# Optimization experiments

Hardware: AMD Instinct MI355X
Metric: run time of the kernel (lower is better)

The kernel has to match this reference:

```python
import jax, jax.numpy as jnp
import numpy as np

J = 4
K = 16  # kernel_size
M_ORDER = 4
PAD = K // 2


def _make_filters():
    t = np.linspace(-2.0, 2.0, K)
    z = 1.0 - 1j * t
    psi = (1.0 / z) ** (M_ORDER + 1)
    psi = psi - psi.mean()
    phi = np.exp(-2.0 * t ** 2)
    phi = phi / phi.sum()
    psi = psi / np.linalg.norm(psi) / np.sqrt(2.0)
    phi = phi / np.linalg.norm(phi) / np.sqrt(2.0)
    return (psi.real.astype(np.float32), psi.imag.astype(np.float32),
            phi.astype(np.float32))


def setup_inputs() -> dict:
    key = jax.random.key(0)
    k1, k2 = jax.random.split(key)
    B, T = 32, 524288
    x_real = jax.random.normal(k1, (B, T), dtype=jnp.float32)
    x_imag = jax.random.normal(k2, (B, T), dtype=jnp.float32)
    pr, pi, ph = _make_filters()
    return {
        'x_real': x_real, 'x_imag': x_imag,
        'psi_real': jnp.asarray(pr), 'psi_imag': jnp.asarray(pi),
        'phi': jnp.asarray(ph),
    }


def _conv_same(x, w, L):
    # x: (B, L) real; w: (K,) real. torch F.conv1d = cross-correlation, 'same'-ish
    # padding K//2 gives length L+1, trimmed back to L (as in the torch code).
    y = jax.lax.conv_general_dilated(x[:, None, :], w[None, None, :],
                                     window_strides=(1,),
                                     padding=[(PAD, PAD)])
    return y[:, 0, :L]


def reference(x_real, x_imag, psi_real, psi_imag, phi):
    x = x_real + 1j * x_imag  # complex64
    coefficients = []
    for j in range(J):
        L = x.shape[-1]
        xr, xi = x.real, x.imag
        # low-pass (complex signal * real filter), then decimate by 2
        s = _conv_same(xr, phi, L) + 1j * _conv_same(xi, phi, L)
        coefficients.append(s[..., ::2])
        # complex band-pass conv: (a+bi)*(c+di)
        rr = _conv_same(xr, psi_real, L)
        ri = _conv_same(xr, psi_imag, L)
        ir = _conv_same(xi, psi_real, L)
        ii = _conv_same(xi, psi_imag, L)
        u = (rr - ii) + 1j * (ri + ir)
        # modulus rectifier (cast back to complex, imag = 0)
        w = jnp.abs(u).astype(u.dtype)
        x = w[..., ::2]
        if x.shape[-1] < K:
            break
    return tuple(coefficients)
```

## Files before the change

### kernel.cpp

```cpp
#include <hip/hip_runtime.h>


using f16x2 = __attribute__((ext_vector_type(2))) __fp16;

static __device__ __forceinline__ uint packh2(float a, float b) {
    f16x2 r = __builtin_amdgcn_cvt_pkrtz(a, b);
    return __builtin_bit_cast(uint, r);
}
static __device__ __forceinline__ float dot2(f16x2 f, uint w, float c) {
#if __has_builtin(__builtin_amdgcn_fdot2)
    return __builtin_amdgcn_fdot2(f, __builtin_bit_cast(f16x2, w), c, false);
#else
    f16x2 h = __builtin_bit_cast(f16x2, w);
    return fmaf((float)f.x, (float)h.x, fmaf((float)f.y, (float)h.y, c));
#endif
}

constexpr int S1   = 1024;
constexpr int H1   = 56;
constexpr int NT1  = S1 + 2 * H1;
constexpr int NPIN = 1144;
constexpr int NLD  = NPIN / 2;
constexpr int NTH  = 256;

__global__ __launch_bounds__(NTH, 6) void hst_fused_kernel(
    const float* __restrict__ xr, const float* __restrict__ xi,
    const float* __restrict__ psi_r, const float* __restrict__ psi_i,
    const float* __restrict__ phi,
    float* __restrict__ out,
    long o0, long o1, long o2, long o3,
    int L0, int h0, int h1, int h2, int h3)
{
    __shared__ __align__(16) uint REP[NPIN];
    __shared__ __align__(16) uint IMP[NPIN];
    __shared__ __align__(16) uint X1P[572];
    __shared__ __align__(16) uint X2P[284];
    __shared__ __align__(16) uint X3P[136];

    const int tid  = threadIdx.x;
    const int wv   = tid >> 6;
    const int lane = tid & 63;
    const int gx   = blockIdx.x;
    const int b    = blockIdx.y;
    const int s    = gx * S1;
    const bool edge = (gx == 0) || (gx == (int)gridDim.x - 1);
    const int X0   = 2 * (s - H1) - 8;

    const float* rowr = xr + (size_t)b * (size_t)L0;
    const float* rowi = xi + (size_t)b * (size_t)L0;

    f16x2 FH[8], FR[8], FI[8];
    #pragma unroll
    for (int j = 0; j < 8; ++j) {
        FH[j] = __builtin_amdgcn_cvt_pkrtz(phi[2*j],   phi[2*j+1]);
        FR[j] = __builtin_amdgcn_cvt_pkrtz(psi_r[2*j], psi_r[2*j+1]);
        FI[j] = __builtin_amdgcn_cvt_pkrtz(psi_i[2*j], psi_i[2*j+1]);
    }

    if (!edge) {
        const float4* pr4 = reinterpret_cast<const float4*>(rowr + X0);
        const float4* pi4 = reinterpret_cast<const float4*>(rowi + X0);
        #pragma unroll
        for (int n = 0; n < 2; ++n) {
            const int i = tid + n * NTH;
            float4 a = pr4[i];
            float4 c = pi4[i];
            uint2 wa; wa.x = packh2(a.x, a.y); wa.y = packh2(a.z, a.w);
            uint2 wc; wc.x = packh2(c.x, c.y); wc.y = packh2(c.z, c.w);
            *reinterpret_cast<uint2*>(&REP[2*i]) = wa;
            *reinterpret_cast<uint2*>(&IMP[2*i]) = wc;
        }
        if (lane < 15) {
            const int i = 512 + 4 * lane + wv;
            if (i < NLD) {
                float4 a = pr4[i];
                float4 c = pi4[i];
                uint2 wa; wa.x = packh2(a.x, a.y); wa.y = packh2(a.z, a.w);
                uint2 wc; wc.x = packh2(c.x, c.y); wc.y = packh2(c.z, c.w);
                *reinterpret_cast<uint2*>(&REP[2*i]) = wa;
                *reinterpret_cast<uint2*>(&IMP[2*i]) = wc;
            }
        }
    } else {
        for (int i = tid; i < NPIN; i += NTH) {
            int g0 = X0 + 2 * i;
            float r0 = (g0   >= 0 && g0   < L0) ? rowr[g0]   : 0.0f;
            float r1 = (g0+1 >= 0 && g0+1 < L0) ? rowr[g0+1] : 0.0f;
            float i0 = (g0   >= 0 && g0   < L0) ? rowi[g0]   : 0.0f;
            float i1 = (g0+1 >= 0 && g0+1 < L0) ? rowi[g0+1] : 0.0f;
            REP[i] = packh2(r0, r1);
            IMP[i] = packh2(i0, i1);
        }
    }
    __syncthreads();

    {
        const int g = tid;
        const uint4* wp = reinterpret_cast<const uint4*>(&REP[4*g]);
        uint4 a0 = wp[0], a1 = wp[1], a2 = wp[2];
        const uint4* ip = reinterpret_cast<const uint4*>(&IMP[4*g]);
        uint4 c0v = ip[0], c1v = ip[1], c2v = ip[2];
        const uint wr[12] = {a0.x,a0.y,a0.z,a0.w, a1.x,a1.y,a1.z,a1.w, a2.x,a2.y,a2.z,a2.w};
        const uint wi[12] = {c0v.x,c0v.y,c0v.z,c0v.w, c1v.x,c1v.y,c1v.z,c1v.w, c2v.x,c2v.y,c2v.z,c2v.w};

        float phv[4], mag[4];
        #pragma unroll
        for (int r = 0; r < 4; ++r) {
            float sh = 0.f, rr = 0.f, ri = 0.f, ir = 0.f, ii = 0.f;
            #pragma unroll
            for (int j = 0; j < 8; ++j) {
                sh = dot2(FH[j], wr[r+j], sh);
                rr = dot2(FR[j], wr[r+j], rr);
                ri = dot2(FI[j], wr[r+j], ri);
                ir = dot2(FR[j], wi[r+j], ir);
                ii = dot2(FI[j], wi[r+j], ii);
            }
            float ur = rr - ii, ui = ri + ir;
            float m2 = sqrtf(fmaf(ur, ur, ui * ui));
            if (edge) {
                int m = s - H1 + 4*g + r;
                m2 = (m >= 0 && m < h0) ? m2 : 0.0f;
            }
            mag[r] = m2;
            phv[r] = sh;
        }
        uint2 xp; xp.x = packh2(mag[0], mag[1]); xp.y = packh2(mag[2], mag[3]);
        *reinterpret_cast<uint2*>(&X1P[2*g]) = xp;

        if (g >= 14) {
            long m0 = (long)s - H1 + 4*g;
            float4 st; st.x = phv[0]; st.y = phv[1]; st.z = phv[2]; st.w = phv[3];
            *reinterpret_cast<float4*>(out + o0 + (long)b * h0 + m0) = st;
        }
    }

    if (lane < 28) {
        const int h  = 4 * lane + wv;
        const int lm = 1024 + h;
        uint wr8[8], wi8[8];
        #pragma unroll
        for (int j = 0; j < 8; ++j) { wr8[j] = REP[lm + j]; wi8[j] = IMP[lm + j]; }
        float sh = 0.f, rr = 0.f, ri = 0.f, ir = 0.f, ii = 0.f;
        #pragma unroll
        for (int j = 0; j < 8; ++j) {
            sh = dot2(FH[j], wr8[j], sh);
            rr = dot2(FR[j], wr8[j], rr);
            ri = dot2(FI[j], wr8[j], ri);
            ir = dot2(FR[j], wi8[j], ir);
            ii = dot2(FI[j], wi8[j], ii);
        }
        float ur = rr - ii, ui = ri + ir;
        float m2 = sqrtf(fmaf(ur, ur, ui * ui));
        if (edge) {
            int m = s - H1 + lm;
            m2 = (m >= 0 && m < h0) ? m2 : 0.0f;
        }
        reinterpret_cast<__fp16*>(X1P)[lm] = (__fp16)m2;
        if (h < 56)
            out[o0 + (long)b * h0 + (s + 968 + h)] = sh;
    }
    __syncthreads();

    {
        const int t = tid;
        uint2 u0 = *reinterpret_cast<const uint2*>(&X1P[2*t]);
        uint2 u1 = *reinterpret_cast<const uint2*>(&X1P[2*t+2]);
        uint2 u2 = *reinterpret_cast<const uint2*>(&X1P[2*t+4]);
        uint2 u3 = *reinterpret_cast<const uint2*>(&X1P[2*t+6]);
        uint  w8 = X1P[2*t+8];
        const uint w[9] = {u0.x,u0.y,u1.x,u1.y,u2.x,u2.y,u3.x,u3.y,w8};

        float phv[2], mag[2];
        #pragma unroll
        for (int r = 0; r < 2; ++r) {
            float sh = 0.f, ur = 0.f, ui = 0.f;
            #pragma unroll
            for (int j = 0; j < 8; ++j) {
                sh = dot2(FH[j], w[r+j], sh);
                ur = dot2(FR[j], w[r+j], ur);
                ui = dot2(FI[j], w[r+j], ui);
            }
            float m2 = sqrtf(fmaf(ur, ur, ui * ui));
            const int q = s/2 - 24 + 2*t + r;
            if (edge) m2 = (q >= 0 && q < h1) ? m2 : 0.0f;
            mag[r] = m2;
            phv[r] = sh;
        }
        X2P[t] = packh2(mag[0], mag[1]);
        if (t >= 12) {
            long q0 = (long)s/2 - 24 + 2*t;
            *reinterpret_cast<float2*>(out + o1 + (long)b * h1 + q0) =
                make_float2(phv[0], phv[1]);
        }
    }
    if (lane < 12) {
        const int h   = 4 * lane + wv;
        const int pos = 512 + h;
        uint w8[8];
        #pragma unroll
        for (int j = 0; j < 8; ++j) w8[j] = X1P[pos + j];
        float sh = 0.f, ur = 0.f, ui = 0.f;
        #pragma unroll
        for (int j = 0; j < 8; ++j) {
            sh = dot2(FH[j], w8[j], sh);
            ur = dot2(FR[j], w8[j], ur);
            ui = dot2(FI[j], w8[j], ui);
        }
        float m2 = sqrtf(fmaf(ur, ur, ui * ui));
        const int q = s/2 - 24 + pos;
        if (edge) m2 = (q >= 0 && q < h1) ? m2 : 0.0f;
        reinterpret_cast<__fp16*>(X2P)[pos] = (__fp16)m2;
        if (h < 24)
            out[o1 + (long)b * h1 + q] = sh;
    }
    __syncthreads();

    if (tid < 136) {
        const int t = tid;
        uint2 u0 = *reinterpret_cast<const uint2*>(&X2P[2*t]);
        uint2 u1 = *reinterpret_cast<const uint2*>(&X2P[2*t+2]);
        uint2 u2 = *reinterpret_cast<const uint2*>(&X2P[2*t+4]);
        uint2 u3 = *reinterpret_cast<const uint2*>(&X2P[2*t+6]);
        uint  w8 = X2P[2*t+8];
        const uint w[9] = {u0.x,u0.y,u1.x,u1.y,u2.x,u2.y,u3.x,u3.y,w8};

        float phv[2], mag[2];
        #pragma unroll
        for (int r = 0; r < 2; ++r) {
            float sh = 0.f, ur = 0.f, ui = 0.f;
            #pragma unroll
            for (int j = 0; j < 8; ++j) {
                sh = dot2(FH[j], w[r+j], sh);
                ur = dot2(FR[j], w[r+j], ur);
                ui = dot2(FI[j], w[r+j], ui);
            }
            float m2 = sqrtf(fmaf(ur, ur, ui * ui));
            const int p = s/4 - 8 + 2*t + r;
            if (edge) m2 = (p >= 0 && p < h2) ? m2 : 0.0f;
            mag[r] = m2;
            phv[r] = sh;
        }
        X3P[t] = packh2(mag[0], mag[1]);
        if (t >= 4 && t < 132) {
            long p0 = (long)s/4 - 8 + 2*t;
            *reinterpret_cast<float2*>(out + o2 + (long)b * h2 + p0) =
                make_float2(phv[0], phv[1]);
        }
    }
    __syncthreads();

    if (tid < S1/8) {
        float sh = 0.f;
        #pragma unroll
        for (int j = 0; j < 8; ++j)
            sh = dot2(FH[j], X3P[tid + j], sh);
        out[o3 + (long)b * h3 + (s/8 + tid)] = sh;
    }
}

extern "C" void kernel_launch(void* const* d_in, const int* in_sizes, int n_in,
                              void* d_out, int out_size, void* d_ws, size_t ws_size,
                              hipStream_t stream) {
    const float* xr    = (const float*)d_in[0];
    const float* xi    = (const float*)d_in[1];
    const float* psi_r = (const float*)d_in[2];
    const float* psi_i = (const float*)d_in[3];
    const float* phi   = (const float*)d_in[4];
    float* out = (float*)d_out;

    const int B  = 32;
    const int T  = in_sizes[0] / B;
    const int L0 = T;
    const int h0 = L0 / 2;
    const int h1 = h0 / 2;
    const int h2 = h1 / 2;
    const int h3 = h2 / 2;

    const long o0 = 0;
    const long o1 = o0 + (long)B * h0;
    const long o2 = o1 + (long)B * h1;
    const long o3 = o2 + (long)B * h2;

    dim3 blk(NTH, 1, 1);
    dim3 grd(h0 / S1, B, 1);
    hipLaunchKernelGGL(hst_fused_kernel, grd, blk, 0, stream,
                       xr, xi, psi_r, psi_i, phi,
                       out, o0, o1, o2, o3,
                       L0, h0, h1, h2, h3);
}
```

Baseline: 49.32 us.

## Double per-block tile to 2048 samples to amortize halo recomputation

Doubles the output tile per block from 1024 to 2048 samples and enlarges the shared buffers, so each thread now computes two groups in level 1 and four outputs in level 2. The halo cost across the cascaded levels (56 at level 1, 24 at level 2, 8 at level 3) is spread over twice as much useful work, cutting redundant loads and recomputation. The tail-handling thread mappings are reworked for the new sizes. In exchange the grid is half as large, and the larger shared memory footprint and register pressure may lower occupancy.

After: 47.37 us. 4.0% less time.

```diff
diff --git a/kernel.cpp b/kernel.cpp
--- a/kernel.cpp
+++ b/kernel.cpp
@@ -16,11 +16,13 @@
 #endif
 }
 
-constexpr int S1   = 1024;
+constexpr int S1   = 2048;
 constexpr int H1   = 56;
 constexpr int NT1  = S1 + 2 * H1;
-constexpr int NPIN = 1144;
+constexpr int NPIN = 2168;
 constexpr int NLD  = NPIN / 2;
+constexpr int NT2  = S1 / 2 + 48;
+constexpr int NT3  = S1 / 4 + 16;
 constexpr int NTH  = 256;
 
 __global__ __launch_bounds__(NTH, 6) void hst_fused_kernel(
@@ -33,9 +35,9 @@
 {
     __shared__ __align__(16) uint REP[NPIN];
     __shared__ __align__(16) uint IMP[NPIN];
-    __shared__ __align__(16) uint X1P[572];
-    __shared__ __align__(16) uint X2P[284];
-    __shared__ __align__(16) uint X3P[136];
+    __shared__ __align__(16) uint X1P[1080];
+    __shared__ __align__(16) uint X2P[536];
+    __shared__ __align__(16) uint X3P[264];
 
     const int tid  = threadIdx.x;
     const int wv   = tid >> 6;
@@ -61,7 +63,7 @@
         const float4* pr4 = reinterpret_cast<const float4*>(rowr + X0);
         const float4* pi4 = reinterpret_cast<const float4*>(rowi + X0);
         #pragma unroll
-        for (int n = 0; n < 2; ++n) {
+        for (int n = 0; n < 4; ++n) {
             const int i = tid + n * NTH;
             float4 a = pr4[i];
             float4 c = pi4[i];
@@ -71,15 +73,13 @@
             *reinterpret_cast<uint2*>(&IMP[2*i]) = wc;
         }
         if (lane < 15) {
-            const int i = 512 + 4 * lane + wv;
-            if (i < NLD) {
-                float4 a = pr4[i];
-                float4 c = pi4[i];
-                uint2 wa; wa.x = packh2(a.x, a.y); wa.y = packh2(a.z, a.w);
-                uint2 wc; wc.x = packh2(c.x, c.y); wc.y = packh2(c.z, c.w);
-                *reinterpret_cast<uint2*>(&REP[2*i]) = wa;
-                *reinterpret_cast<uint2*>(&IMP[2*i]) = wc;
-            }
+            const int i = 1024 + 15 * wv + lane;
+            float4 a = pr4[i];
+            float4 c = pi4[i];
+            uint2 wa; wa.x = packh2(a.x, a.y); wa.y = packh2(a.z, a.w);
+            uint2 wc; wc.x = packh2(c.x, c.y); wc.y = packh2(c.z, c.w);
+            *reinterpret_cast<uint2*>(&REP[2*i]) = wa;
+            *reinterpret_cast<uint2*>(&IMP[2*i]) = wc;
         }
     } else {
         for (int i = tid; i < NPIN; i += NTH) {
@@ -94,8 +94,9 @@
     }
     __syncthreads();
 
-    {
-        const int g = tid;
+    #pragma unroll
+    for (int n = 0; n < 2; ++n) {
+        const int g = tid + n * NTH;
         const uint4* wp = reinterpret_cast<const uint4*>(&REP[4*g]);
         uint4 a0 = wp[0], a1 = wp[1], a2 = wp[2];
         const uint4* ip = reinterpret_cast<const uint4*>(&IMP[4*g]);
@@ -135,8 +136,8 @@
     }
 
     if (lane < 28) {
-        const int h  = 4 * lane + wv;
-        const int lm = 1024 + h;
+        const int h  = 28 * wv + lane;
+        const int lm = S1 + h;
         uint wr8[8], wi8[8];
         #pragma unroll
         for (int j = 0; j < 8; ++j) { wr8[j] = REP[lm + j]; wi8[j] = IMP[lm + j]; }
@@ -157,22 +158,21 @@
         }
         reinterpret_cast<__fp16*>(X1P)[lm] = (__fp16)m2;
         if (h < 56)
-            out[o0 + (long)b * h0 + (s + 968 + h)] = sh;
+            out[o0 + (long)b * h0 + (s + S1 - H1 + h)] = sh;
     }
     __syncthreads();
 
     {
         const int t = tid;
-        uint2 u0 = *reinterpret_cast<const uint2*>(&X1P[2*t]);
-        uint2 u1 = *reinterpret_cast<const uint2*>(&X1P[2*t+2]);
-        uint2 u2 = *reinterpret_cast<const uint2*>(&X1P[2*t+4]);
-        uint2 u3 = *reinterpret_cast<const uint2*>(&X1P[2*t+6]);
-        uint  w8 = X1P[2*t+8];
-        const uint w[9] = {u0.x,u0.y,u1.x,u1.y,u2.x,u2.y,u3.x,u3.y,w8};
-
-        float phv[2], mag[2];
-        #pragma unroll
-        for (int r = 0; r < 2; ++r) {
+        const uint4* wp = reinterpret_cast<const uint4*>(&X1P[4*t]);
+        uint4 a0 = wp[0], a1 = wp[1];
+        uint2 u2 = *reinterpret_cast<const uint2*>(&X1P[4*t+8]);
+        uint  w10 = X1P[4*t+10];
+        const uint w[11] = {a0.x,a0.y,a0.z,a0.w, a1.x,a1.y,a1.z,a1.w, u2.x,u2.y, w10};
+
+        float phv[4], mag[4];
+        #pragma unroll
+        for (int r = 0; r < 4; ++r) {
             float sh = 0.f, ur = 0.f, ui = 0.f;
             #pragma unroll
             for (int j = 0; j < 8; ++j) {
@@ -181,21 +181,23 @@
                 ui = dot2(FI[j], w[r+j], ui);
             }
             float m2 = sqrtf(fmaf(ur, ur, ui * ui));
-            const int q = s/2 - 24 + 2*t + r;
+            const int q = s/2 - 24 + 4*t + r;
             if (edge) m2 = (q >= 0 && q < h1) ? m2 : 0.0f;
             mag[r] = m2;
             phv[r] = sh;
         }
-        X2P[t] = packh2(mag[0], mag[1]);
-        if (t >= 12) {
-            long q0 = (long)s/2 - 24 + 2*t;
-            *reinterpret_cast<float2*>(out + o1 + (long)b * h1 + q0) =
-                make_float2(phv[0], phv[1]);
+        uint2 xp; xp.x = packh2(mag[0], mag[1]); xp.y = packh2(mag[2], mag[3]);
+        *reinterpret_cast<uint2*>(&X2P[2*t]) = xp;
+
+        if (t >= 6) {
+            long q0 = (long)s/2 - 24 + 4*t;
+            float4 st; st.x = phv[0]; st.y = phv[1]; st.z = phv[2]; st.w = phv[3];
+            *reinterpret_cast<float4*>(out + o1 + (long)b * h1 + q0) = st;
         }
     }
     if (lane < 12) {
-        const int h   = 4 * lane + wv;
-        const int pos = 512 + h;
+        const int h   = 12 * wv + lane;
+        const int pos = 1024 + h;
         uint w8[8];
         #pragma unroll
         for (int j = 0; j < 8; ++j) w8[j] = X1P[pos + j];
@@ -215,7 +217,7 @@
     }
     __syncthreads();
 
-    if (tid < 136) {
+    {
         const int t = tid;
         uint2 u0 = *reinterpret_cast<const uint2*>(&X2P[2*t]);
         uint2 u1 = *reinterpret_cast<const uint2*>(&X2P[2*t+2]);
@@ -241,15 +243,35 @@
             phv[r] = sh;
         }
         X3P[t] = packh2(mag[0], mag[1]);
-        if (t >= 4 && t < 132) {
+        if (t >= 4) {
             long p0 = (long)s/4 - 8 + 2*t;
             *reinterpret_cast<float2*>(out + o2 + (long)b * h2 + p0) =
                 make_float2(phv[0], phv[1]);
         }
     }
+    if (lane < 4) {
+        const int h   = 4 * wv + lane;
+        const int pos = 512 + h;
+        uint w8[8];
+        #pragma unroll
+        for (int j = 0; j < 8; ++j) w8[j] = X2P[pos + j];
+        float sh = 0.f, ur = 0.f, ui = 0.f;
+        #pragma unroll
+        for (int j = 0; j < 8; ++j) {
+            sh = dot2(FH[j], w8[j], sh);
+            ur = dot2(FR[j], w8[j], ur);
+            ui = dot2(FI[j], w8[j], ui);
+        }
+        float m2 = sqrtf(fmaf(ur, ur, ui * ui));
+        const int p = s/4 - 8 + pos;
+        if (edge) m2 = (p >= 0 && p < h2) ? m2 : 0.0f;
+        reinterpret_cast<__fp16*>(X3P)[pos] = (__fp16)m2;
+        if (h < 8)
+            out[o2 + (long)b * h2 + p] = sh;
+    }
     __syncthreads();
 
-    if (tid < S1/8) {
+    {
         float sh = 0.f;
         #pragma unroll
         for (int j = 0; j < 8; ++j)
```
